# Performance work log

Hardware: AMD Instinct MI355X
Metric: run time of the kernel (lower is better)

The kernel has to match this reference:

```python
import jax, jax.numpy as jnp
import numpy as np

B, T, H, N_IN, N_OUT = 256, 1024, 512, 64, 64


def setup_inputs() -> dict:
    key = jax.random.key(0)
    k_x, k_w, k_win, k_wout = jax.random.split(key, 4)
    # nn.Linear(in, out, bias=False) weight has shape [out, in]
    X = jax.random.normal(k_x, (B, T, N_IN), dtype=jnp.float32)
    h0 = jnp.zeros((B, H), dtype=jnp.float32)
    W = jax.random.normal(k_w, (H, H), dtype=jnp.float32) / np.sqrt(H)
    W_in = jax.random.normal(k_win, (H, N_IN), dtype=jnp.float32) / np.sqrt(N_IN)
    W_out = jax.random.normal(k_wout, (N_OUT, H), dtype=jnp.float32) / np.sqrt(H)
    return {"X": X, "h0": h0, "W": W, "W_in": W_in, "W_out": W_out}


def reference(X, h0, W, W_in, W_out):
    # Precompute input projections for all timesteps in one big GEMM:
    # inp[b, t, h] = X[b, t, :] @ W_in.T  (same math as per-step W_in(x_t))
    inp = jnp.einsum("bti,hi->tbh", X, W_in)  # [T, B, H]

    def step(h, inp_t):
        h_next = jnp.tanh(h) @ W.T + inp_t  # [B, H]
        return h_next, h_next

    _, hidden = jax.lax.scan(step, h0, inp)  # hidden: [T, B, H]
    hidden = jnp.transpose(hidden, (1, 0, 2))  # [B, T, H]
    out = jnp.einsum("bth,oh->bto", hidden, W_out)  # [B, T, n_out]
    return out, hidden
```

## Files before the change

kernel.cpp:

```cpp
#include <hip/hip_runtime.h>
#include <stdint.h>

#define B_    256
#define T_    1024
#define H_    512
#define NIN_  64
#define NOUT_ 64

#define SC_NW   8
#define BBLK    4
#define HROW    528
#define KB_AG   8
#define KB_ST   4
#define KB_LD   4
#define LD_U    (KB_LD * 4)
#define SW_CHUNKS (SC_NW * KB_ST * 4 * 64)

typedef __attribute__((ext_vector_type(8))) short bf16x8;
typedef __attribute__((ext_vector_type(4))) float f32x4;

__device__ __forceinline__ short f2bf(float f) {
  uint32_t u = __float_as_uint(f);
  uint32_t r = (u + 0x7FFFu + ((u >> 16) & 1u)) >> 16;
  return (short)(r & 0xFFFFu);
}

__device__ __forceinline__ bf16x8 pack8(float4 lo, float4 hi) {
  bf16x8 s;
  s[0] = f2bf(lo.x); s[1] = f2bf(lo.y); s[2] = f2bf(lo.z); s[3] = f2bf(lo.w);
  s[4] = f2bf(hi.x); s[5] = f2bf(hi.y); s[6] = f2bf(hi.z); s[7] = f2bf(hi.w);
  return s;
}

__device__ __forceinline__ float fast_tanh(float x) {
  float e = __expf(2.0f * x);
  return 1.0f - __fdividef(2.0f, e + 1.0f);
}

__device__ __forceinline__ void mfma4_agpr(
    f32x4& d0, f32x4& d1, f32x4& d2, f32x4& d3, bf16x8 a,
    const bf16x8& b0, const bf16x8& b1, const bf16x8& b2, const bf16x8& b3) {
  asm volatile(
      "v_mfma_f32_16x16x32_bf16 %0, %4, %5, %0\n\t"
      "v_mfma_f32_16x16x32_bf16 %1, %4, %6, %1\n\t"
      "v_mfma_f32_16x16x32_bf16 %2, %4, %7, %2\n\t"
      "v_mfma_f32_16x16x32_bf16 %3, %4, %8, %3\n\t"
      "s_nop 7"
      : "+v"(d0), "+v"(d1), "+v"(d2), "+v"(d3)
      : "v"(a), "a"(b0), "a"(b1), "a"(b2), "a"(b3));
}

__global__ __launch_bounds__(512) void wprep(
    const float* __restrict__ W, short* __restrict__ sw)
{
  const int c = blockIdx.x * 512 + threadIdx.x;
  if (c >= SW_CHUNKS) return;
  const int lane = c & 63;
  const int u    = c >> 6;
  const int jt   = u & 3;
  const int gw   = u >> 2;
  const int G    = gw & 3;
  const int w    = gw >> 2;
  const int col  = 64 * w + 16 * jt + (lane & 15);
  const int k0   = 32 * (KB_AG + G) + (lane >> 4) * 8;
  const float4* p = reinterpret_cast<const float4*>(W + (size_t)col * H_ + k0);
  *reinterpret_cast<bf16x8*>(sw + (size_t)c * 8) = pack8(p[0], p[1]);
}

#define XP_BLOCKS 512
__global__ __launch_bounds__(512, 2) void xproj(
    const float* __restrict__ X, const float* __restrict__ Win,
    float* __restrict__ inp)
{
  const int tid  = threadIdx.x;
  const int lane = tid & 63;
  const int w    = tid >> 6;
  const int g    = lane >> 4;
  const int m    = lane & 15;

  bf16x8 Bf[2][4];
#pragma unroll
  for (int kb = 0; kb < 2; ++kb)
#pragma unroll
    for (int jt = 0; jt < 4; ++jt) {
      const int j = 64 * w + 16 * jt + m;
      const float4* p = reinterpret_cast<const float4*>(Win + (size_t)j * NIN_ + 32 * kb + 8 * g);
      Bf[kb][jt] = pack8(p[0], p[1]);
    }

  const int NTILES = (B_ * T_) / 16;
  const f32x4 zero = {0.f, 0.f, 0.f, 0.f};

  for (int tile = blockIdx.x; tile < NTILES; tile += XP_BLOCKS) {
    const size_t row0 = (size_t)tile * 16;
    f32x4 acc[4];
    {
      const float4* p = reinterpret_cast<const float4*>(X + (row0 + m) * NIN_ + 8 * g);
      const bf16x8 a = pack8(p[0], p[1]);
#pragma unroll
      for (int jt = 0; jt < 4; ++jt)
        acc[jt] = __builtin_amdgcn_mfma_f32_16x16x32_bf16(a, Bf[0][jt], zero, 0, 0, 0);
    }
    {
      const float4* p = reinterpret_cast<const float4*>(X + (row0 + m) * NIN_ + 32 + 8 * g);
      const bf16x8 a = pack8(p[0], p[1]);
#pragma unroll
      for (int jt = 0; jt < 4; ++jt)
        acc[jt] = __builtin_amdgcn_mfma_f32_16x16x32_bf16(a, Bf[1][jt], acc[jt], 0, 0, 0);
    }
#pragma unroll
    for (int jt = 0; jt < 4; ++jt)
#pragma unroll
      for (int r = 0; r < 4; ++r)
        inp[(row0 + 4 * g + r) * H_ + 64 * w + 16 * jt + m] = acc[jt][r];
  }
}

__global__
__attribute__((amdgpu_flat_work_group_size(512, 512), amdgpu_waves_per_eu(2, 2)))
void rnn_scan(
    const float* __restrict__ h0, const float* __restrict__ W,
    float* __restrict__ hid, const short* __restrict__ swbuf)
{
  __shared__ __align__(16) short wlds[SC_NW * LD_U * 64 * 8];
  __shared__ __align__(16) short hbuf[2][BBLK][HROW];

  const int tid  = threadIdx.x;
  const int lane = tid & 63;
  const int w    = tid >> 6;
  const int g    = lane >> 4;
  const int m    = lane & 15;
  const int b0   = blockIdx.x * BBLK;

  const float* Wo = W;
  asm volatile("" : "+s"(Wo));
  const short* SWb = swbuf;
  asm volatile("" : "+s"(SWb));

  bf16x8 Wa[KB_AG][4];
#pragma unroll
  for (int kb = 0; kb < KB_AG; ++kb)
#pragma unroll
    for (int jt = 0; jt < 4; ++jt) {
      const int col = 64 * w + 16 * jt + m;
      const float4* p = reinterpret_cast<const float4*>(Wo + (size_t)col * H_ + 32 * kb + 8 * g);
      Wa[kb][jt] = pack8(p[0], p[1]);
    }

#pragma unroll
  for (int i = 0; i < 16; ++i) {
    const int c  = tid + 512 * i;
    const int l  = c & 63;
    const int u  = (c >> 6) & 15;
    const int ww = c >> 10;
    const int kb = 12 + (u >> 2);
    const int jt = u & 3;
    const int col = 64 * ww + 16 * jt + (l & 15);
    const int k0  = 32 * kb + (l >> 4) * 8;
    const float4* p = reinterpret_cast<const float4*>(Wo + (size_t)col * H_ + k0);
    *reinterpret_cast<bf16x8*>(&wlds[((size_t)(ww * LD_U + u) * 64 + l) * 8]) = pack8(p[0], p[1]);
  }

  for (int e = tid; e < BBLK * H_; e += SC_NW * 64) {
    const int r = e >> 9, k = e & (H_ - 1);
    hbuf[0][r][k] = f2bf(fast_tanh(h0[(size_t)(b0 + r) * H_ + k]));
  }

  const int mycol = 64 * w + 16 * g + m;
  float inp_cur[4];
#pragma unroll
  for (int r = 0; r < 4; ++r)
    inp_cur[r] = hid[((size_t)(b0 + r) * T_ + 0) * H_ + mycol];

  const int sbase = (w * KB_ST * 4) * 64 + lane;
  const bf16x8* SW = reinterpret_cast<const bf16x8*>(SWb);
  bf16x8 sb0[4], sb1[4];
#pragma unroll
  for (int jt = 0; jt < 4; ++jt) sb0[jt] = SW[sbase + (0 * 4 + jt) * 64];
#pragma unroll
  for (int jt = 0; jt < 4; ++jt) sb1[jt] = SW[sbase + (1 * 4 + jt) * 64];

  __syncthreads();

#pragma clang loop unroll(disable)
  for (int t = 0; t < T_; ++t) {
    const int cur = t & 1, nxt = cur ^ 1;

    uintptr_t swo_u = (uintptr_t)SW;
    asm volatile("" : "+s"(swo_u));
    const bf16x8* SWo = (const bf16x8*)swo_u;

    float inp_nxt[4] = {0.f, 0.f, 0.f, 0.f};
    if (t + 1 < T_) {
#pragma unroll
      for (int r = 0; r < 4; ++r)
        inp_nxt[r] = hid[((size_t)(b0 + r) * T_ + (t + 1)) * H_ + mycol];
    }

    const short* hr = &hbuf[cur][m & 3][0];
    f32x4 acc[4];

    {
      const bf16x8 a = *reinterpret_cast<const bf16x8*>(hr + 32 * 8 + 8 * g);
      const f32x4 zero = {0.f, 0.f, 0.f, 0.f};
#pragma unroll
      for (int jt = 0; jt < 4; ++jt)
        acc[jt] = __builtin_amdgcn_mfma_f32_16x16x32_bf16(a, sb0[jt], zero, 0, 0, 0);
#pragma unroll
      for (int jt = 0; jt < 4; ++jt) sb0[jt] = SWo[sbase + (2 * 4 + jt) * 64];
    }

#pragma unroll
    for (int kb = 0; kb < KB_AG; ++kb) {
      const bf16x8 a = *reinterpret_cast<const bf16x8*>(hr + 32 * kb + 8 * g);
      mfma4_agpr(acc[0], acc[1], acc[2], acc[3], a,
                 Wa[kb][0], Wa[kb][1], Wa[kb][2], Wa[kb][3]);
    }

    {
      const bf16x8 a = *reinterpret_cast<const bf16x8*>(hr + 32 * 9 + 8 * g);
#pragma unroll
      for (int jt = 0; jt < 4; ++jt)
        acc[jt] = __builtin_amdgcn_mfma_f32_16x16x32_bf16(a, sb1[jt], acc[jt], 0, 0, 0);
#pragma unroll
      for (int jt = 0; jt < 4; ++jt) sb1[jt] = SWo[sbase + (3 * 4 + jt) * 64];
    }

#pragma unroll
    for (int kk = 0; kk < 2; ++kk) {
      const int kb = 12 + kk;
      const bf16x8 a = *reinterpret_cast<const bf16x8*>(hr + 32 * kb + 8 * g);
#pragma unroll
      for (int jt = 0; jt < 4; ++jt) {
        const bf16x8 b = *reinterpret_cast<const bf16x8*>(
            &wlds[((size_t)(w * LD_U + kk * 4 + jt) * 64 + lane) * 8]);
        acc[jt] = __builtin_amdgcn_mfma_f32_16x16x32_bf16(a, b, acc[jt], 0, 0, 0);
      }
    }

    {
      const bf16x8 a = *reinterpret_cast<const bf16x8*>(hr + 32 * 10 + 8 * g);
#pragma unroll
      for (int jt = 0; jt < 4; ++jt)
        acc[jt] = __builtin_amdgcn_mfma_f32_16x16x32_bf16(a, sb0[jt], acc[jt], 0, 0, 0);
#pragma unroll
      for (int jt = 0; jt < 4; ++jt) sb0[jt] = SWo[sbase + (0 * 4 + jt) * 64];
    }

#pragma unroll
    for (int kk = 2; kk < 4; ++kk) {
      const int kb = 12 + kk;
      const bf16x8 a = *reinterpret_cast<const bf16x8*>(hr + 32 * kb + 8 * g);
#pragma unroll
      for (int jt = 0; jt < 4; ++jt) {
        const bf16x8 b = *reinterpret_cast<const bf16x8*>(
            &wlds[((size_t)(w * LD_U + kk * 4 + jt) * 64 + lane) * 8]);
        acc[jt] = __builtin_amdgcn_mfma_f32_16x16x32_bf16(a, b, acc[jt], 0, 0, 0);
      }
    }

    {
      const bf16x8 a = *reinterpret_cast<const bf16x8*>(hr + 32 * 11 + 8 * g);
#pragma unroll
      for (int jt = 0; jt < 4; ++jt)
        acc[jt] = __builtin_amdgcn_mfma_f32_16x16x32_bf16(a, sb1[jt], acc[jt], 0, 0, 0);
#pragma unroll
      for (int jt = 0; jt < 4; ++jt) sb1[jt] = SWo[sbase + (1 * 4 + jt) * 64];
    }

#pragma unroll
    for (int r = 0; r < 4; ++r) {
      float v = acc[0][r];
      v = (g == 1) ? acc[1][r] : v;
      v = (g == 2) ? acc[2][r] : v;
      v = (g == 3) ? acc[3][r] : v;
      v += inp_cur[r];
      hid[((size_t)(b0 + r) * T_ + t) * H_ + mycol] = v;
      hbuf[nxt][r][mycol] = f2bf(fast_tanh(v));
    }
#pragma unroll
    for (int r = 0; r < 4; ++r) inp_cur[r] = inp_nxt[r];

    asm volatile("s_waitcnt lgkmcnt(0)" ::: "memory");
    __builtin_amdgcn_s_barrier();
    asm volatile("" ::: "memory");
  }
}

#define OP_BLOCKS 1024
#define OP_WAVES  8
__global__ __launch_bounds__(OP_WAVES * 64, 2) void out_proj(
    const float* __restrict__ hid, const float* __restrict__ Wout,
    float* __restrict__ out)
{
  __shared__ __align__(16) short ws[16][NOUT_][32];

  const int tid  = threadIdx.x;
  const int lane = tid & 63;
  const int w    = tid >> 6;
  const int g    = lane >> 4;
  const int m    = lane & 15;

#pragma unroll
  for (int i = 0; i < 8; ++i) {
    const int c   = tid + OP_WAVES * 64 * i;
    const int kb  = c >> 8;
    const int col = (c >> 2) & 63;
    const int q   = (c & 3) * 8;
    const float4* p = reinterpret_cast<const float4*>(Wout + (size_t)col * H_ + 32 * kb + q);
    *reinterpret_cast<bf16x8*>(&ws[kb][col][q]) = pack8(p[0], p[1]);
  }
  __syncthreads();

  const int wave_id = blockIdx.x * OP_WAVES + w;
  const int NWAVES  = OP_BLOCKS * OP_WAVES;
  const int NTILES  = (B_ * T_) / 16;

  for (int tile = wave_id; tile < NTILES; tile += NWAVES) {
    const size_t row0 = (size_t)tile * 16;
    f32x4 acc[4];
    {
      const float4* p = reinterpret_cast<const float4*>(hid + (row0 + m) * H_ + 8 * g);
      const bf16x8 a = pack8(p[0], p[1]);
      const f32x4 zero = {0.f, 0.f, 0.f, 0.f};
#pragma unroll
      for (int jt = 0; jt < 4; ++jt) {
        const bf16x8 b = *reinterpret_cast<const bf16x8*>(&ws[0][16 * jt + m][8 * g]);
        acc[jt] = __builtin_amdgcn_mfma_f32_16x16x32_bf16(a, b, zero, 0, 0, 0);
      }
    }
#pragma unroll
    for (int kb = 1; kb < 16; ++kb) {
      const float4* p = reinterpret_cast<const float4*>(hid + (row0 + m) * H_ + 32 * kb + 8 * g);
      const bf16x8 a = pack8(p[0], p[1]);
#pragma unroll
      for (int jt = 0; jt < 4; ++jt) {
        const bf16x8 b = *reinterpret_cast<const bf16x8*>(&ws[kb][16 * jt + m][8 * g]);
        acc[jt] = __builtin_amdgcn_mfma_f32_16x16x32_bf16(a, b, acc[jt], 0, 0, 0);
      }
    }
#pragma unroll
    for (int jt = 0; jt < 4; ++jt)
#pragma unroll
      for (int r = 0; r < 4; ++r)
        out[(row0 + 4 * g + r) * NOUT_ + 16 * jt + m] = acc[jt][r];
  }
}

extern "C" void kernel_launch(void* const* d_in, const int* in_sizes, int n_in,
                              void* d_out, int out_size, void* d_ws, size_t ws_size,
                              hipStream_t stream) {
  const float* X    = (const float*)d_in[0];
  const float* h0   = (const float*)d_in[1];
  const float* W    = (const float*)d_in[2];
  const float* Win  = (const float*)d_in[3];
  const float* Wout = (const float*)d_in[4];

  float* out = (float*)d_out;
  float* hid = (float*)d_out + (size_t)B_ * T_ * NOUT_;

  const size_t out_elems = (size_t)B_ * T_ * NOUT_;
  short* sw = (short*)((float*)d_out + out_elems) - (size_t)SW_CHUNKS * 8;

  wprep<<<dim3(SW_CHUNKS / 512), dim3(512), 0, stream>>>(W, sw);
  xproj<<<dim3(XP_BLOCKS), dim3(512), 0, stream>>>(X, Win, hid);
  rnn_scan<<<dim3(B_ / BBLK), dim3(SC_NW * 64), 0, stream>>>(h0, W, hid, sw);
  out_proj<<<dim3(OP_BLOCKS), dim3(OP_WAVES * 64), 0, stream>>>(hid, Wout, out);
}
```

Measured before the change: 2.855 ms.

## Stream all non-register W k-blocks from global instead of LDS

Removes the LDS-resident copy of W k-blocks 12-15 and instead streams all eight non-AGPR k-blocks (8-15) from the prepacked bf16 global buffer, using four rotating register sets. The intent is to cut LDS read traffic and LDS footprint in the per-timestep loop and to interleave global prefetches with the AGPR MFMAs for better latency hiding. In exchange it doubles per-step global/L2 weight traffic and adds 16 more VGPR-resident bf16x8 values, which could raise register pressure at the enforced two waves per EU.

```diff
diff --git a/kernel.cpp b/kernel.cpp
--- a/kernel.cpp
+++ b/kernel.cpp
@@ -11,9 +11,7 @@
 #define BBLK    4
 #define HROW    528
 #define KB_AG   8
-#define KB_ST   4
-#define KB_LD   4
-#define LD_U    (KB_LD * 4)
+#define KB_ST   8
 #define SW_CHUNKS (SC_NW * KB_ST * 4 * 64)
 
 typedef __attribute__((ext_vector_type(8))) short bf16x8;
@@ -59,8 +57,8 @@
   const int u    = c >> 6;
   const int jt   = u & 3;
   const int gw   = u >> 2;
-  const int G    = gw & 3;
-  const int w    = gw >> 2;
+  const int G    = gw & 7;
+  const int w    = gw >> 3;
   const int col  = 64 * w + 16 * jt + (lane & 15);
   const int k0   = 32 * (KB_AG + G) + (lane >> 4) * 8;
   const float4* p = reinterpret_cast<const float4*>(W + (size_t)col * H_ + k0);
@@ -122,7 +120,6 @@
     const float* __restrict__ h0, const float* __restrict__ W,
     float* __restrict__ hid, const short* __restrict__ swbuf)
 {
-  __shared__ __align__(16) short wlds[SC_NW * LD_U * 64 * 8];
   __shared__ __align__(16) short hbuf[2][BBLK][HROW];
 
   const int tid  = threadIdx.x;
@@ -147,20 +144,6 @@
       Wa[kb][jt] = pack8(p[0], p[1]);
     }
 
-#pragma unroll
-  for (int i = 0; i < 16; ++i) {
-    const int c  = tid + 512 * i;
-    const int l  = c & 63;
-    const int u  = (c >> 6) & 15;
-    const int ww = c >> 10;
-    const int kb = 12 + (u >> 2);
-    const int jt = u & 3;
-    const int col = 64 * ww + 16 * jt + (l & 15);
-    const int k0  = 32 * kb + (l >> 4) * 8;
-    const float4* p = reinterpret_cast<const float4*>(Wo + (size_t)col * H_ + k0);
-    *reinterpret_cast<bf16x8*>(&wlds[((size_t)(ww * LD_U + u) * 64 + l) * 8]) = pack8(p[0], p[1]);
-  }
-
   for (int e = tid; e < BBLK * H_; e += SC_NW * 64) {
     const int r = e >> 9, k = e & (H_ - 1);
     hbuf[0][r][k] = f2bf(fast_tanh(h0[(size_t)(b0 + r) * H_ + k]));
@@ -172,13 +155,17 @@
   for (int r = 0; r < 4; ++r)
     inp_cur[r] = hid[((size_t)(b0 + r) * T_ + 0) * H_ + mycol];
 
-  const int sbase = (w * KB_ST * 4) * 64 + lane;
+  const int sbase = w * (KB_ST * 4 * 64) + lane;
   const bf16x8* SW = reinterpret_cast<const bf16x8*>(SWb);
-  bf16x8 sb0[4], sb1[4];
+  bf16x8 sb0[4], sb1[4], sb2[4], sb3[4];
 #pragma unroll
   for (int jt = 0; jt < 4; ++jt) sb0[jt] = SW[sbase + (0 * 4 + jt) * 64];
 #pragma unroll
   for (int jt = 0; jt < 4; ++jt) sb1[jt] = SW[sbase + (1 * 4 + jt) * 64];
+#pragma unroll
+  for (int jt = 0; jt < 4; ++jt) sb2[jt] = SW[sbase + (2 * 4 + jt) * 64];
+#pragma unroll
+  for (int jt = 0; jt < 4; ++jt) sb3[jt] = SW[sbase + (3 * 4 + jt) * 64];
 
   __syncthreads();
 
@@ -207,65 +194,87 @@
       for (int jt = 0; jt < 4; ++jt)
         acc[jt] = __builtin_amdgcn_mfma_f32_16x16x32_bf16(a, sb0[jt], zero, 0, 0, 0);
 #pragma unroll
-      for (int jt = 0; jt < 4; ++jt) sb0[jt] = SWo[sbase + (2 * 4 + jt) * 64];
-    }
-
-#pragma unroll
-    for (int kb = 0; kb < KB_AG; ++kb) {
+      for (int jt = 0; jt < 4; ++jt) sb0[jt] = SWo[sbase + (4 * 4 + jt) * 64];
+    }
+#pragma unroll
+    for (int kb = 0; kb < 2; ++kb) {
       const bf16x8 a = *reinterpret_cast<const bf16x8*>(hr + 32 * kb + 8 * g);
       mfma4_agpr(acc[0], acc[1], acc[2], acc[3], a,
                  Wa[kb][0], Wa[kb][1], Wa[kb][2], Wa[kb][3]);
     }
-
     {
       const bf16x8 a = *reinterpret_cast<const bf16x8*>(hr + 32 * 9 + 8 * g);
 #pragma unroll
       for (int jt = 0; jt < 4; ++jt)
         acc[jt] = __builtin_amdgcn_mfma_f32_16x16x32_bf16(a, sb1[jt], acc[jt], 0, 0, 0);
 #pragma unroll
-      for (int jt = 0; jt < 4; ++jt) sb1[jt] = SWo[sbase + (3 * 4 + jt) * 64];
-    }
-
-#pragma unroll
-    for (int kk = 0; kk < 2; ++kk) {
-      const int kb = 12 + kk;
+      for (int jt = 0; jt < 4; ++jt) sb1[jt] = SWo[sbase + (5 * 4 + jt) * 64];
+    }
+#pragma unroll
+    for (int kb = 2; kb < 4; ++kb) {
       const bf16x8 a = *reinterpret_cast<const bf16x8*>(hr + 32 * kb + 8 * g);
-#pragma unroll
-      for (int jt = 0; jt < 4; ++jt) {
-        const bf16x8 b = *reinterpret_cast<const bf16x8*>(
-            &wlds[((size_t)(w * LD_U + kk * 4 + jt) * 64 + lane) * 8]);
-        acc[jt] = __builtin_amdgcn_mfma_f32_16x16x32_bf16(a, b, acc[jt], 0, 0, 0);
-      }
-    }
-
+      mfma4_agpr(acc[0], acc[1], acc[2], acc[3], a,
+                 Wa[kb][0], Wa[kb][1], Wa[kb][2], Wa[kb][3]);
+    }
     {
       const bf16x8 a = *reinterpret_cast<const bf16x8*>(hr + 32 * 10 + 8 * g);
 #pragma unroll
       for (int jt = 0; jt < 4; ++jt)
+        acc[jt] = __builtin_amdgcn_mfma_f32_16x16x32_bf16(a, sb2[jt], acc[jt], 0, 0, 0);
+#pragma unroll
+      for (int jt = 0; jt < 4; ++jt) sb2[jt] = SWo[sbase + (6 * 4 + jt) * 64];
+    }
+#pragma unroll
+    for (int kb = 4; kb < 6; ++kb) {
+      const bf16x8 a = *reinterpret_cast<const bf16x8*>(hr + 32 * kb + 8 * g);
+      mfma4_agpr(acc[0], acc[1], acc[2], acc[3], a,
+                 Wa[kb][0], Wa[kb][1], Wa[kb][2], Wa[kb][3]);
+    }
+    {
+      const bf16x8 a = *reinterpret_cast<const bf16x8*>(hr + 32 * 11 + 8 * g);
+#pragma unroll
+      for (int jt = 0; jt < 4; ++jt)
+        acc[jt] = __builtin_amdgcn_mfma_f32_16x16x32_bf16(a, sb3[jt], acc[jt], 0, 0, 0);
+#pragma unroll
+      for (int jt = 0; jt < 4; ++jt) sb3[jt] = SWo[sbase + (7 * 4 + jt) * 64];
+    }
+#pragma unroll
+    for (int kb = 6; kb < 8; ++kb) {
+      const bf16x8 a = *reinterpret_cast<const bf16x8*>(hr + 32 * kb + 8 * g);
+      mfma4_agpr(acc[0], acc[1], acc[2], acc[3], a,
+                 Wa[kb][0], Wa[kb][1], Wa[kb][2], Wa[kb][3]);
+    }
+    {
+      const bf16x8 a = *reinterpret_cast<const bf16x8*>(hr + 32 * 12 + 8 * g);
+#pragma unroll
+      for (int jt = 0; jt < 4; ++jt)
         acc[jt] = __builtin_amdgcn_mfma_f32_16x16x32_bf16(a, sb0[jt], acc[jt], 0, 0, 0);
 #pragma unroll
       for (int jt = 0; jt < 4; ++jt) sb0[jt] = SWo[sbase + (0 * 4 + jt) * 64];
     }
-
-#pragma unroll
-    for (int kk = 2; kk < 4; ++kk) {
-      const int kb = 12 + kk;
-      const bf16x8 a = *reinterpret_cast<const bf16x8*>(hr + 32 * kb + 8 * g);
-#pragma unroll
-      for (int jt = 0; jt < 4; ++jt) {
-        const bf16x8 b = *reinterpret_cast<const bf16x8*>(
-            &wlds[((size_t)(w * LD_U + kk * 4 + jt) * 64 + lane) * 8]);
-        acc[jt] = __builtin_amdgcn_mfma_f32_16x16x32_bf16(a, b, acc[jt], 0, 0, 0);
-      }
-    }
-
-    {
-      const bf16x8 a = *reinterpret_cast<const bf16x8*>(hr + 32 * 11 + 8 * g);
+    {
+      const bf16x8 a = *reinterpret_cast<const bf16x8*>(hr + 32 * 13 + 8 * g);
 #pragma unroll
       for (int jt = 0; jt < 4; ++jt)
         acc[jt] = __builtin_amdgcn_mfma_f32_16x16x32_bf16(a, sb1[jt], acc[jt], 0, 0, 0);
 #pragma unroll
       for (int jt = 0; jt < 4; ++jt) sb1[jt] = SWo[sbase + (1 * 4 + jt) * 64];
+    }
+    {
+      const bf16x8 a = *reinterpret_cast<const bf16x8*>(hr + 32 * 14 + 8 * g);
+#pragma unroll
+      for (int jt = 0; jt < 4; ++jt)
+        acc[jt] = __builtin_amdgcn_mfma_f32_16x16x32_bf16(a, sb2[jt], acc[jt], 0, 0, 0);
+#pragma unroll
+      for (int jt = 0; jt < 4; ++jt) sb2[jt] = SWo[sbase + (2 * 4 + jt) * 64];
+    }
+    {
+      const bf16x8 a = *reinterpret_cast<const bf16x8*>(hr + 32 * 15 + 8 * g);
+#pragma unroll
+      for (int jt = 0; jt < 4; ++jt)
+        acc[jt] = __builtin_amdgcn_mfma_f32_16x16x32_bf16(a, sb3[jt], acc[jt], 0, 0, 0);
+#pragma unroll
+      for (int jt = 0; jt < 4; ++jt) sb3[jt] = SWo[sbase + (3 * 4 + jt) * 64];
     }
 
 #pragma unroll
```

Result: slower. 4.141 ms (+45.0%).
